# Kernel optimization log

Hardware: AMD Instinct MI355X
Metric: run time of the kernel (lower is better)

The kernel has to match this reference:

```python
import jax, jax.numpy as jnp
import numpy as np

# q4_0: blocks of 32 weights; per block: 2-byte fp16 scale 'd' + 16 packed bytes
# (element i in low nibble of byte i, element i+16 in high nibble). value = d*(q-8).
SHAPE = (8192, 8192)
NUMEL = SHAPE[0] * SHAPE[1]
QK = 32
NBLOCKS = NUMEL // QK          # 2_097_152
BLOCK_BYTES = 18               # 2 (fp16 scale) + 16 (packed nibbles)


def setup_inputs() -> dict:
    rng = np.random.default_rng(0)
    w = (rng.standard_normal((NBLOCKS, QK)) * 0.02).astype(np.float32)
    # faithful q4_0 requantization (ggml): d = signed max-magnitude value / -8
    amax_idx = np.argmax(np.abs(w), axis=1)
    maxv = w[np.arange(NBLOCKS), amax_idx]
    d = (maxv / -8.0).astype(np.float16)
    inv_d = np.where(d != 0, 1.0 / d.astype(np.float32), 0.0)
    q = np.clip(np.rint(w * inv_d[:, None]) + 8.0, 0, 15).astype(np.uint8)
    packed = (q[:, :16] | (q[:, 16:] << 4)).astype(np.uint8)     # [NB,16]
    scale_bytes = d.view(np.uint8).reshape(NBLOCKS, 2)            # little-endian fp16 bits
    raw = np.concatenate([scale_bytes, packed], axis=1).reshape(-1)  # [NB*18] uint8
    return {"raw_data": jnp.asarray(raw)}


def reference(raw_data) -> jnp.ndarray:
    raw = raw_data.reshape(NBLOCKS, BLOCK_BYTES)
    # reassemble fp16 scale from two little-endian bytes
    s16 = raw[:, 0].astype(jnp.uint16) | (raw[:, 1].astype(jnp.uint16) << 8)
    scale = jax.lax.bitcast_convert_type(s16, jnp.float16).astype(jnp.float32)  # [NB]
    qs = raw[:, 2:]                                   # [NB,16] packed nibbles
    lo = (qs & 0xF).astype(jnp.float32)               # elements 0..15
    hi = (qs >> 4).astype(jnp.float32)                # elements 16..31
    q = jnp.concatenate([lo, hi], axis=1) - 8.0       # [NB,32]
    return (scale[:, None] * q).reshape(SHAPE)
```

## Files before the change

kernel.cpp:

```cpp
#include <hip/hip_runtime.h>
#include <hip/hip_fp16.h>


constexpr long long NUMEL = 8192LL * 8192LL;
constexpr int QK = 32;
constexpr long long NBLOCKS = NUMEL / QK;
constexpr int BLOCK_INTS = 18;

__global__ __launch_bounds__(256)
void dequant_q4_kernel(const int* __restrict__ raw32,
                       float4* __restrict__ out4)
{
    const int t = blockIdx.x * 256 + threadIdx.x;
    const int b = t >> 3;
    const int k = t & 7;

    const int base = b * BLOCK_INTS;

    const int s_lo = raw32[base]     & 0xff;
    const int s_hi = raw32[base + 1] & 0xff;
    const unsigned short s16 = (unsigned short)(s_lo | (s_hi << 8));
    const float scale = __half2float(__ushort_as_half(s16));

    const int j = (k & 3) * 4;
    const int2 q01 = *(const int2*)(raw32 + base + 2 + j);
    const int2 q23 = *(const int2*)(raw32 + base + 2 + j + 2);

    const int sh = (k >= 4) ? 4 : 0;

    float4 o;
    o.x = scale * (float)(((q01.x >> sh) & 15) - 8);
    o.y = scale * (float)(((q01.y >> sh) & 15) - 8);
    o.z = scale * (float)(((q23.x >> sh) & 15) - 8);
    o.w = scale * (float)(((q23.y >> sh) & 15) - 8);

    out4[t] = o;
}

extern "C" void kernel_launch(void* const* d_in, const int* in_sizes, int n_in,
                              void* d_out, int out_size, void* d_ws, size_t ws_size,
                              hipStream_t stream)
{
    const int* raw32 = (const int*)d_in[0];
    float4* out4 = (float4*)d_out;

    const long long n_threads = NUMEL / 4;
    const int block = 256;
    const long long grid = n_threads / block;

    dequant_q4_kernel<<<dim3((unsigned)grid), dim3(block), 0, stream>>>(raw32, out4);
}
```

Measured before the change: 353.7 us.

## Stage each workgroup's quant blocks in LDS via coalesced int4 loads

Each 256-thread workgroup now covers 32 q4_0 blocks. It first copies their contiguous 576 ints from global memory into shared memory using int4 loads from 144 threads, then synchronises. Each thread then reads its scale and nibble words from LDS, replacing the earlier overlapping, partly redundant per-thread int2 global reads. This aims to make input traffic fully coalesced and vector-wide. The cost is a barrier per workgroup and idle threads during staging.

```diff
diff --git a/kernel.cpp b/kernel.cpp
--- a/kernel.cpp
+++ b/kernel.cpp
@@ -6,25 +6,35 @@
 constexpr int QK = 32;
 constexpr long long NBLOCKS = NUMEL / QK;
 constexpr int BLOCK_INTS = 18;
+constexpr int WG_BLOCKS = 32;
+constexpr int WG_INTS = WG_BLOCKS * BLOCK_INTS;
 
 __global__ __launch_bounds__(256)
 void dequant_q4_kernel(const int* __restrict__ raw32,
                        float4* __restrict__ out4)
 {
-    const int t = blockIdx.x * 256 + threadIdx.x;
-    const int b = t >> 3;
-    const int k = t & 7;
+    __shared__ int lds[WG_INTS];
 
-    const int base = b * BLOCK_INTS;
+    const int tid = threadIdx.x;
+    const long long wg = blockIdx.x;
 
-    const int s_lo = raw32[base]     & 0xff;
-    const int s_hi = raw32[base + 1] & 0xff;
-    const unsigned short s16 = (unsigned short)(s_lo | (s_hi << 8));
+    if (tid < WG_INTS / 4) {
+        const int4 v = *(const int4*)(raw32 + wg * WG_INTS + (long long)tid * 4);
+        ((int4*)lds)[tid] = v;
+    }
+    __syncthreads();
+
+    const int bl = tid >> 3;
+    const int k  = tid & 7;
+    const int base = bl * BLOCK_INTS;
+
+    const int2 s = *(const int2*)(lds + base);
+    const unsigned short s16 = (unsigned short)((s.x & 0xff) | ((s.y & 0xff) << 8));
     const float scale = __half2float(__ushort_as_half(s16));
 
     const int j = (k & 3) * 4;
-    const int2 q01 = *(const int2*)(raw32 + base + 2 + j);
-    const int2 q23 = *(const int2*)(raw32 + base + 2 + j + 2);
+    const int2 q01 = *(const int2*)(lds + base + 2 + j);
+    const int2 q23 = *(const int2*)(lds + base + 4 + j);
 
     const int sh = (k >= 4) ? 4 : 0;
 
@@ -34,7 +44,7 @@
     o.z = scale * (float)(((q23.x >> sh) & 15) - 8);
     o.w = scale * (float)(((q23.y >> sh) & 15) - 8);
 
-    out4[t] = o;
+    out4[wg * 256 + tid] = o;
 }
 
 extern "C" void kernel_launch(void* const* d_in, const int* in_sizes, int n_in,
@@ -44,9 +54,6 @@
     const int* raw32 = (const int*)d_in[0];
     float4* out4 = (float4*)d_out;
 
-    const long long n_threads = NUMEL / 4;
-    const int block = 256;
-    const long long grid = n_threads / block;
-
-    dequant_q4_kernel<<<dim3((unsigned)grid), dim3(block), 0, stream>>>(raw32, out4);
+    const long long n_wg = NBLOCKS / WG_BLOCKS;
+    dequant_q4_kernel<<<dim3((unsigned)n_wg), dim3(256), 0, stream>>>(raw32, out4);
 }
```

New measurement: 352.0 us. About the same (-0.5%).
